# Performance work log

Measured on AMD Instinct MI355X. Metric: run time of the kernel, lower is better.

The kernel has to match this reference:

```python
import jax, jax.numpy as jnp
import numpy as np

B, C, H, W = 4, 64, 64, 64
CQ = C // 2

def setup_inputs() -> dict:
    key = jax.random.key(0)
    ks = jax.random.split(key, 7)
    return {
        "x":  jax.random.normal(ks[0], (B, C, H, W), dtype=jnp.float32),
        "Wq": jax.random.normal(ks[1], (CQ, C), dtype=jnp.float32) * 0.05,
        "bq": jax.random.normal(ks[2], (CQ,), dtype=jnp.float32) * 0.05,
        "Wk": jax.random.normal(ks[3], (CQ, C), dtype=jnp.float32) * 0.05,
        "bk": jax.random.normal(ks[4], (CQ,), dtype=jnp.float32) * 0.05,
        "Wl": jax.random.normal(ks[5], (C, C), dtype=jnp.float32) * 0.05,
        "bl": jax.random.normal(ks[6], (C,), dtype=jnp.float32) * 0.05,
    }

def reference(x, Wq, bq, Wk, bk, Wl, bl):
    b, c, h, w = x.shape
    hw = h * w
    xf = x.reshape(b, c, hw)                                   # [B,C,HW]
    # 1x1 convs == per-pixel linear projections
    q = jnp.einsum('oc,bci->boi', Wq, xf) + bq[None, :, None]  # [B,CQ,HW]
    k = jnp.einsum('oc,bci->boi', Wk, xf) + bk[None, :, None]  # [B,CQ,HW]
    # energy[b,i,j] = <q[:,i], k[:,j]>  (proj_query permuted to [B,HW,CQ])
    energy = jnp.einsum('bci,bcj->bij', q, k)                  # [B,HW,HW]
    attn = jax.nn.softmax(energy, axis=-1)                     # softmax over last dim (keys j)
    # torch.bmm(proj_value, attention): out[b,c,j] = sum_i value[b,c,i] * attn[b,i,j]
    out = jnp.einsum('bci,bij->bcj', xf, attn)                 # [B,C,HW]
    out = out.reshape(b, c, h, w)
    out = jnp.einsum('oc,bchw->bohw', Wl, out) + bl[None, :, None, None]
    return out + x
```

## Files before the change

### kernel.cpp

```cpp
#include <hip/hip_runtime.h>
#include <hip/hip_bf16.h>


#define HW 4096
#define BN 4
#define CD 64
#define ISPL 8
#define LOG2E 1.44269504f

typedef short bf16x8 __attribute__((ext_vector_type(8)));
typedef float f32x4 __attribute__((ext_vector_type(4)));

static __device__ inline unsigned bfbits(float f) {
    union { float f; unsigned u; } v{f};
    return (v.u + 0x8000u) >> 16;
}
static __device__ inline float b2f(short s) {
    unsigned u = ((unsigned)(unsigned short)s) << 16;
    float f; __builtin_memcpy(&f, &u, 4); return f;
}
static __device__ inline int cvtpk(float lo, float hi) {
    __hip_bfloat162 h = __float22bfloat162_rn(make_float2(lo, hi));
    int r; __builtin_memcpy(&r, &h, 4); return r;
}
static __device__ inline void gl16(const void* g, void* l) {
    __builtin_amdgcn_global_load_lds(
        (const __attribute__((address_space(1))) unsigned int*)g,
        (__attribute__((address_space(3))) unsigned int*)l, 16, 0, 0);
}



__global__ __launch_bounds__(256, 4) void k_proj(
    const float* __restrict__ x, const float* __restrict__ Wq, const float* __restrict__ bq,
    const float* __restrict__ Wk, const float* __restrict__ bk, const float* __restrict__ Wl,
    short* __restrict__ Qt, short* __restrict__ Kt, short* __restrict__ Yc)
{
    __shared__ __align__(16) char sm[18944];
    short* WcL   = (short*)sm;
    short* xT    = (short*)(sm + 16384);
    float* biasL = (float*)(sm + 18432);

    int t = threadIdx.x;
    int wv = t >> 6, l = t & 63, g = l >> 4, n = l & 15;

    {
        int row = t >> 1, half = t & 1;
        const float* src; float scale = 1.f;
        if (row < 32)      { src = Wq + row * CD; scale = LOG2E; }
        else if (row < 64) { src = Wk + (row - 32) * CD; }
        else               { src = Wl + (row - 64) * CD; }
        int pk[16];
#pragma unroll
        for (int e = 0; e < 16; ++e)
            pk[e] = cvtpk(src[half * 32 + 2 * e] * scale, src[half * 32 + 2 * e + 1] * scale);
#pragma unroll
        for (int q = 0; q < 4; ++q)
            *(int4*)(WcL + row * 64 + ((((half << 2) + q) ^ (row & 7)) << 3)) =
                make_int4(pk[4 * q], pk[4 * q + 1], pk[4 * q + 2], pk[4 * q + 3]);
        if (half == 0)
            biasL[row] = (row < 32) ? LOG2E * bq[row] : (row < 64) ? bk[row - 32] : 0.f;
    }
    int pix0 = blockIdx.x << 4;
    {
        int c = t >> 2, q = t & 3;
        int b = pix0 >> 12, pxb = pix0 & (HW - 1);
        float4 v = *(const float4*)(x + ((size_t)b << 18) + ((size_t)c << 12) + pxb + q * 4);
        float vv[4] = {v.x, v.y, v.z, v.w};
#pragma unroll
        for (int e = 0; e < 4; ++e) {
            int px = q * 4 + e;
            xT[px * 64 + (((c >> 3) ^ (px & 7)) << 3) + (c & 7)] = (short)bfbits(vv[e]);
        }
    }
    __syncthreads();

    bf16x8 B0 = *(const bf16x8*)(xT + n * 64 + ((g ^ (n & 7)) << 3));
    bf16x8 B1 = *(const bf16x8*)(xT + n * 64 + (((4 + g) ^ (n & 7)) << 3));
    int pg = pix0 + n;
#pragma unroll
    for (int mm = 0; mm < 2; ++mm) {
        int mt = wv * 2 + mm;
        bf16x8 A0 = *(const bf16x8*)(WcL + (mt * 16 + n) * 64 + ((g ^ (n & 7)) << 3));
        bf16x8 A1 = *(const bf16x8*)(WcL + (mt * 16 + n) * 64 + (((4 + g) ^ (n & 7)) << 3));
        f32x4 d = {0.f, 0.f, 0.f, 0.f};
        d = __builtin_amdgcn_mfma_f32_16x16x32_bf16(A0, B0, d, 0, 0, 0);
        d = __builtin_amdgcn_mfma_f32_16x16x32_bf16(A1, B1, d, 0, 0, 0);
        d += *(const f32x4*)(biasL + mt * 16 + g * 4);
        if (mt < 4) {
            short* dst = (mt < 2 ? Qt : Kt) + ((size_t)pg << 5) + ((mt & 1) << 4) + (g << 2);
            *(int2*)dst = make_int2(cvtpk(d[0], d[1]), cvtpk(d[2], d[3]));
        } else {
            int ch2 = (mt - 4) * 16 + g * 4;
            int bb = pg >> 12, ii = pg & (HW - 1);
#pragma unroll
            for (int r = 0; r < 4; ++r)
                Yc[(((size_t)(bb * CD + ch2 + r)) << 12) + ii] = (short)bfbits(d[r]);
        }
    }
}


__global__ __launch_bounds__(256, 4) void k_pass1m(
    const short* __restrict__ Qt, const short* __restrict__ Kt, float* __restrict__ mrow)
{
    __shared__ float red[4][16];
    int t = threadIdx.x;
    int wv = t >> 6, l = t & 63, g = l >> 4, n = l & 15;
    int ch = blockIdx.x;
    int b = ch & 3, i0 = (ch >> 2) * 16;
    size_t bHW = (size_t)b << 12;

    bf16x8 aq = *(const bf16x8*)(Qt + ((bHW + i0 + n) << 5) + (g << 3));
    f32x4 ls = {0.f, 0.f, 0.f, 0.f};
    const short* kbase = Kt + ((bHW + wv * 1024 + n) << 5) + (g << 3);
#pragma unroll 8
    for (int jt = 0; jt < 64; ++jt) {
        bf16x8 bk = *(const bf16x8*)(kbase + jt * 512);
        f32x4 z = {0.f, 0.f, 0.f, 0.f};
        f32x4 s = __builtin_amdgcn_mfma_f32_16x16x32_bf16(aq, bk, z, 0, 0, 0);
        ls[0] += exp2f(s[0]); ls[1] += exp2f(s[1]);
        ls[2] += exp2f(s[2]); ls[3] += exp2f(s[3]);
    }
#pragma unroll
    for (int msk = 1; msk < 16; msk <<= 1) {
        ls[0] += __shfl_xor(ls[0], msk, 64);
        ls[1] += __shfl_xor(ls[1], msk, 64);
        ls[2] += __shfl_xor(ls[2], msk, 64);
        ls[3] += __shfl_xor(ls[3], msk, 64);
    }
    if (n == 0) {
#pragma unroll
        for (int r = 0; r < 4; ++r) red[wv][g * 4 + r] = ls[r];
    }
    __syncthreads();
    if (t < 16) {
        float s = red[0][t] + red[1][t] + red[2][t] + red[3][t];
        mrow[bHW + i0 + t] = -log2f(s);
    }
}


__global__ __launch_bounds__(256, 4) void k_pass2(
    const short* __restrict__ Qt, const short* __restrict__ Kt,
    const short* __restrict__ Yc, const float* __restrict__ mrow,
    short* __restrict__ Opart)
{
    __shared__ __align__(16) char smem[36864];
    short* QtL = (short*)smem;
    short* W2L = (short*)(smem + 8192);
    short* Pb  = (short*)(smem + 24576);
    float* MtA = (float*)(smem + 34816);

    int t = threadIdx.x;
    int wv = t >> 6, l = t & 63, g = l >> 4, n = l & 15;
    int ch = blockIdx.x;
    int b = ch >> 8, isp = (ch >> 5) & 7, jt = ch & 31;
    int j0 = jt * 128 + wv * 32;
    size_t bHW = (size_t)b << 12;
    short* Pw = Pb + wv * 1280;

    bf16x8 bk0 = *(const bf16x8*)(Kt + ((bHW + j0 + n) << 5) + (g << 3));
    bf16x8 bk1 = *(const bf16x8*)(Kt + ((bHW + j0 + 16 + n) << 5) + (g << 3));

    f32x4 oacc[2][4];
#pragma unroll
    for (int a = 0; a < 2; ++a)
#pragma unroll
        for (int m = 0; m < 4; ++m) oacc[a][m] = (f32x4){0.f, 0.f, 0.f, 0.f};

    int swz = ((t & 7) ^ ((t >> 3) & 7)) << 4;
    const char* qsrc = (const char*)Qt + ((bHW + (size_t)isp * 512) << 6) + t * 16;
    const char* wsrc = (const char*)Yc + (((size_t)(b * CD + (t >> 3)) << 12) + isp * 512) * 2 + swz;
    char* qd0 = (char*)QtL + t * 16;  char* qd1 = qd0 + 4096;
    char* wd0 = (char*)W2L + t * 16;  char* wd1 = wd0 + 8192;

    gl16(qsrc, qd0);
    gl16(wsrc, wd0);
    gl16(wsrc + (32ull << 13), wd0 + 4096);
    if (t < 128)
        gl16((const char*)(mrow + bHW + (size_t)isp * 512) + t * 16, (char*)MtA + t * 16);
    asm volatile("s_waitcnt vmcnt(0)" ::: "memory");
    __builtin_amdgcn_s_barrier();
    __builtin_amdgcn_sched_barrier(0);

    const int NT = 8;
    for (int st = 0; st < NT; ++st) {
        int cur = st & 1;
        if (st > 0) {
            __builtin_amdgcn_s_barrier();
            __builtin_amdgcn_sched_barrier(0);
        }
        if (st + 1 < NT) {
            gl16(qsrc + (size_t)(st + 1) * 4096, cur ? qd0 : qd1);
            gl16(wsrc + (size_t)(st + 1) * 128, cur ? wd0 : wd1);
            gl16(wsrc + (size_t)(st + 1) * 128 + (32ull << 13), (cur ? wd0 : wd1) + 4096);
            asm volatile("s_waitcnt vmcnt(3)" ::: "memory");
        } else {
            asm volatile("s_waitcnt vmcnt(0)" ::: "memory");
        }
        __builtin_amdgcn_sched_barrier(0);

        const short* qL = QtL + cur * 2048;
        const char* wL = (const char*)W2L + cur * 8192;
        const float* mL = MtA + st * 64;
#pragma unroll
        for (int ks = 0; ks < 2; ++ks) {
            bf16x8 aq0 = *(const bf16x8*)(qL + (ks * 32 + n) * 32 + g * 8);
            bf16x8 aq1 = *(const bf16x8*)(qL + (ks * 32 + 16 + n) * 32 + g * 8);
            f32x4 cm0 = *(const f32x4*)(mL + ks * 32 + g * 4);
            f32x4 cm1 = *(const f32x4*)(mL + ks * 32 + 16 + g * 4);
            __builtin_amdgcn_s_setprio(1);
            f32x4 s00 = __builtin_amdgcn_mfma_f32_16x16x32_bf16(aq0, bk0, cm0, 0, 0, 0);
            f32x4 s01 = __builtin_amdgcn_mfma_f32_16x16x32_bf16(aq1, bk0, cm1, 0, 0, 0);
            f32x4 s10 = __builtin_amdgcn_mfma_f32_16x16x32_bf16(aq0, bk1, cm0, 0, 0, 0);
            f32x4 s11 = __builtin_amdgcn_mfma_f32_16x16x32_bf16(aq1, bk1, cm1, 0, 0, 0);
            __builtin_amdgcn_s_setprio(0);
            *(int2*)(Pw + n * 40 + 4 * g) =
                make_int2(cvtpk(exp2f(s00[0]), exp2f(s00[1])), cvtpk(exp2f(s00[2]), exp2f(s00[3])));
            *(int2*)(Pw + n * 40 + 16 + 4 * g) =
                make_int2(cvtpk(exp2f(s01[0]), exp2f(s01[1])), cvtpk(exp2f(s01[2]), exp2f(s01[3])));
            *(int2*)(Pw + (16 + n) * 40 + 4 * g) =
                make_int2(cvtpk(exp2f(s10[0]), exp2f(s10[1])), cvtpk(exp2f(s10[2]), exp2f(s10[3])));
            *(int2*)(Pw + (16 + n) * 40 + 16 + 4 * g) =
                make_int2(cvtpk(exp2f(s11[0]), exp2f(s11[1])), cvtpk(exp2f(s11[2]), exp2f(s11[3])));
            bf16x8 pb0 = *(const bf16x8*)(Pw + n * 40 + 8 * g);
            bf16x8 pb1 = *(const bf16x8*)(Pw + (16 + n) * 40 + 8 * g);
            __builtin_amdgcn_s_setprio(1);
#pragma unroll
            for (int mb = 0; mb < 4; ++mb) {
                bf16x8 aw = *(const bf16x8*)(wL + (mb * 16 + n) * 128 + ((((ks << 2) + g) ^ (n & 7)) << 4));
                oacc[0][mb] = __builtin_amdgcn_mfma_f32_16x16x32_bf16(aw, pb0, oacc[0][mb], 0, 0, 0);
                oacc[1][mb] = __builtin_amdgcn_mfma_f32_16x16x32_bf16(aw, pb1, oacc[1][mb], 0, 0, 0);
            }
            __builtin_amdgcn_s_setprio(0);
        }
        __builtin_amdgcn_sched_barrier(0);
    }
    size_t obase = ((((size_t)isp * BN + b) * CD) << 12) + j0 + n;
#pragma unroll
    for (int j2 = 0; j2 < 2; ++j2)
#pragma unroll
        for (int mb = 0; mb < 4; ++mb)
#pragma unroll
            for (int r = 0; r < 4; ++r)
                Opart[obase + (((size_t)(mb * 16 + g * 4 + r)) << 12) + j2 * 16] =
                    (short)bfbits(oacc[j2][mb][r]);
}


__global__ __launch_bounds__(256, 4) void k_merge(
    const short* __restrict__ Opart, const float* __restrict__ x,
    const float* __restrict__ bl, float* __restrict__ out)
{
    int t = threadIdx.x;
    int e = (blockIdx.x * 256 + t) * 4;
    int c = (e >> 12) & 63;
    float4 r = *(const float4*)(x + e);
    float bc = bl[c];
    r.x += bc; r.y += bc; r.z += bc; r.w += bc;
#pragma unroll
    for (int p = 0; p < ISPL; ++p) {
        int2 o4 = *(const int2*)(Opart + ((size_t)p << 20) + e);
        r.x += b2f((short)(o4.x & 0xffff));
        r.y += b2f((short)(o4.x >> 16));
        r.z += b2f((short)(o4.y & 0xffff));
        r.w += b2f((short)(o4.y >> 16));
    }
    *(float4*)(out + e) = r;
}

extern "C" void kernel_launch(void* const* d_in, const int* in_sizes, int n_in,
                              void* d_out, int out_size, void* d_ws, size_t ws_size,
                              hipStream_t stream)
{
    (void)in_sizes; (void)n_in; (void)out_size; (void)ws_size;
    const float* x  = (const float*)d_in[0];
    const float* Wq = (const float*)d_in[1];
    const float* bq = (const float*)d_in[2];
    const float* Wk = (const float*)d_in[3];
    const float* bk = (const float*)d_in[4];
    const float* Wl = (const float*)d_in[5];
    const float* bl = (const float*)d_in[6];
    float* out = (float*)d_out;
    char* base = (char*)d_ws;

    short* Qt    = (short*)(base);
    short* Kt    = (short*)(base + 0x100000);
    short* Yc    = (short*)(base + 0x200000);
    float* mrow  = (float*)(base + 0x500000);
    short* Opart = (short*)(base + 0x510000);

    hipLaunchKernelGGL(k_proj, dim3(1024), dim3(256), 0, stream,
                       x, Wq, bq, Wk, bk, Wl, Qt, Kt, Yc);
    hipLaunchKernelGGL(k_pass1m, dim3(1024), dim3(256), 0, stream, Qt, Kt, mrow);
    hipLaunchKernelGGL(k_pass2, dim3(1024), dim3(256), 0, stream,
                       Qt, Kt, Yc, mrow, Opart);
    hipLaunchKernelGGL(k_merge, dim3(1024), dim3(256), 0, stream, Opart, x, bl, out);
}
```

Baseline: 63.98 us.

## Halve i-split count and double rows per pass1 block to reuse K loads

New measurement: 65.61 us. +2.6%, slower.

```diff
diff --git a/kernel.cpp b/kernel.cpp
--- a/kernel.cpp
+++ b/kernel.cpp
@@ -5,7 +5,7 @@
 #define HW 4096
 #define BN 4
 #define CD 64
-#define ISPL 8
+#define ISPL 4
 #define LOG2E 1.44269504f
 
 typedef short bf16x8 __attribute__((ext_vector_type(8)));
@@ -104,37 +104,45 @@
 __global__ __launch_bounds__(256, 4) void k_pass1m(
     const short* __restrict__ Qt, const short* __restrict__ Kt, float* __restrict__ mrow)
 {
-    __shared__ float red[4][16];
+    __shared__ float red[4][32];
     int t = threadIdx.x;
     int wv = t >> 6, l = t & 63, g = l >> 4, n = l & 15;
     int ch = blockIdx.x;
-    int b = ch & 3, i0 = (ch >> 2) * 16;
+    int b = ch & 3, i0 = (ch >> 2) * 32;
     size_t bHW = (size_t)b << 12;
 
-    bf16x8 aq = *(const bf16x8*)(Qt + ((bHW + i0 + n) << 5) + (g << 3));
-    f32x4 ls = {0.f, 0.f, 0.f, 0.f};
+    bf16x8 aq0 = *(const bf16x8*)(Qt + ((bHW + i0 + n) << 5) + (g << 3));
+    bf16x8 aq1 = *(const bf16x8*)(Qt + ((bHW + i0 + 16 + n) << 5) + (g << 3));
+    f32x4 ls0 = {0.f, 0.f, 0.f, 0.f}, ls1 = {0.f, 0.f, 0.f, 0.f};
     const short* kbase = Kt + ((bHW + wv * 1024 + n) << 5) + (g << 3);
-#pragma unroll 8
+#pragma unroll 4
     for (int jt = 0; jt < 64; ++jt) {
-        bf16x8 bk = *(const bf16x8*)(kbase + jt * 512);
+        bf16x8 bkv = *(const bf16x8*)(kbase + jt * 512);
         f32x4 z = {0.f, 0.f, 0.f, 0.f};
-        f32x4 s = __builtin_amdgcn_mfma_f32_16x16x32_bf16(aq, bk, z, 0, 0, 0);
-        ls[0] += exp2f(s[0]); ls[1] += exp2f(s[1]);
-        ls[2] += exp2f(s[2]); ls[3] += exp2f(s[3]);
+        f32x4 s0 = __builtin_amdgcn_mfma_f32_16x16x32_bf16(aq0, bkv, z, 0, 0, 0);
+        f32x4 s1 = __builtin_amdgcn_mfma_f32_16x16x32_bf16(aq1, bkv, z, 0, 0, 0);
+        ls0[0] += exp2f(s0[0]); ls0[1] += exp2f(s0[1]);
+        ls0[2] += exp2f(s0[2]); ls0[3] += exp2f(s0[3]);
+        ls1[0] += exp2f(s1[0]); ls1[1] += exp2f(s1[1]);
+        ls1[2] += exp2f(s1[2]); ls1[3] += exp2f(s1[3]);
     }
 #pragma unroll
     for (int msk = 1; msk < 16; msk <<= 1) {
-        ls[0] += __shfl_xor(ls[0], msk, 64);
-        ls[1] += __shfl_xor(ls[1], msk, 64);
-        ls[2] += __shfl_xor(ls[2], msk, 64);
-        ls[3] += __shfl_xor(ls[3], msk, 64);
+#pragma unroll
+        for (int r = 0; r < 4; ++r) {
+            ls0[r] += __shfl_xor(ls0[r], msk, 64);
+            ls1[r] += __shfl_xor(ls1[r], msk, 64);
+        }
     }
     if (n == 0) {
 #pragma unroll
-        for (int r = 0; r < 4; ++r) red[wv][g * 4 + r] = ls[r];
+        for (int r = 0; r < 4; ++r) {
+            red[wv][g * 4 + r] = ls0[r];
+            red[wv][16 + g * 4 + r] = ls1[r];
+        }
     }
     __syncthreads();
-    if (t < 16) {
+    if (t < 32) {
         float s = red[0][t] + red[1][t] + red[2][t] + red[3][t];
         mrow[bHW + i0 + t] = -log2f(s);
     }
@@ -146,7 +154,7 @@
     const short* __restrict__ Yc, const float* __restrict__ mrow,
     short* __restrict__ Opart)
 {
-    __shared__ __align__(16) char smem[36864];
+    __shared__ __align__(16) char smem[38912];
     short* QtL = (short*)smem;
     short* W2L = (short*)(smem + 8192);
     short* Pb  = (short*)(smem + 24576);
@@ -155,7 +163,7 @@
     int t = threadIdx.x;
     int wv = t >> 6, l = t & 63, g = l >> 4, n = l & 15;
     int ch = blockIdx.x;
-    int b = ch >> 8, isp = (ch >> 5) & 7, jt = ch & 31;
+    int b = ch >> 7, isp = (ch >> 5) & 3, jt = ch & 31;
     int j0 = jt * 128 + wv * 32;
     size_t bHW = (size_t)b << 12;
     short* Pw = Pb + wv * 1280;
@@ -170,21 +178,20 @@
         for (int m = 0; m < 4; ++m) oacc[a][m] = (f32x4){0.f, 0.f, 0.f, 0.f};
 
     int swz = ((t & 7) ^ ((t >> 3) & 7)) << 4;
-    const char* qsrc = (const char*)Qt + ((bHW + (size_t)isp * 512) << 6) + t * 16;
-    const char* wsrc = (const char*)Yc + (((size_t)(b * CD + (t >> 3)) << 12) + isp * 512) * 2 + swz;
+    const char* qsrc = (const char*)Qt + ((bHW + (size_t)isp * 1024) << 6) + t * 16;
+    const char* wsrc = (const char*)Yc + (((size_t)(b * CD + (t >> 3)) << 12) + isp * 1024) * 2 + swz;
     char* qd0 = (char*)QtL + t * 16;  char* qd1 = qd0 + 4096;
     char* wd0 = (char*)W2L + t * 16;  char* wd1 = wd0 + 8192;
 
     gl16(qsrc, qd0);
     gl16(wsrc, wd0);
     gl16(wsrc + (32ull << 13), wd0 + 4096);
-    if (t < 128)
-        gl16((const char*)(mrow + bHW + (size_t)isp * 512) + t * 16, (char*)MtA + t * 16);
+    gl16((const char*)(mrow + bHW + (size_t)isp * 1024) + t * 16, (char*)MtA + t * 16);
     asm volatile("s_waitcnt vmcnt(0)" ::: "memory");
     __builtin_amdgcn_s_barrier();
     __builtin_amdgcn_sched_barrier(0);
 
-    const int NT = 8;
+    const int NT = 16;
     for (int st = 0; st < NT; ++st) {
         int cur = st & 1;
         if (st > 0) {
@@ -293,8 +300,8 @@
 
     hipLaunchKernelGGL(k_proj, dim3(1024), dim3(256), 0, stream,
                        x, Wq, bq, Wk, bk, Wl, Qt, Kt, Yc);
-    hipLaunchKernelGGL(k_pass1m, dim3(1024), dim3(256), 0, stream, Qt, Kt, mrow);
-    hipLaunchKernelGGL(k_pass2, dim3(1024), dim3(256), 0, stream,
+    hipLaunchKernelGGL(k_pass1m, dim3(512), dim3(256), 0, stream, Qt, Kt, mrow);
+    hipLaunchKernelGGL(k_pass2, dim3(512), dim3(256), 0, stream,
                        Qt, Kt, Yc, mrow, Opart);
     hipLaunchKernelGGL(k_merge, dim3(1024), dim3(256), 0, stream, Opart, x, bl, out);
 }
```

## Tile pass1 over 64 query rows with double-buffered LDS staging of keys

Applied to the files above, without the earlier changes.

Result: slower. 69.33 us (+8.4%).

```diff
diff --git a/kernel.cpp b/kernel.cpp
--- a/kernel.cpp
+++ b/kernel.cpp
@@ -104,38 +104,89 @@
 __global__ __launch_bounds__(256, 4) void k_pass1m(
     const short* __restrict__ Qt, const short* __restrict__ Kt, float* __restrict__ mrow)
 {
-    __shared__ float red[4][16];
+    __shared__ __align__(16) char sm1[33792];
+    short* KL  = (short*)sm1;
+    float* red = (float*)(sm1 + 32768);
+
     int t = threadIdx.x;
     int wv = t >> 6, l = t & 63, g = l >> 4, n = l & 15;
     int ch = blockIdx.x;
-    int b = ch & 3, i0 = (ch >> 2) * 16;
+    int b = ch & 3, i0 = (ch >> 2) << 6;
     size_t bHW = (size_t)b << 12;
 
-    bf16x8 aq = *(const bf16x8*)(Qt + ((bHW + i0 + n) << 5) + (g << 3));
-    f32x4 ls = {0.f, 0.f, 0.f, 0.f};
-    const short* kbase = Kt + ((bHW + wv * 1024 + n) << 5) + (g << 3);
-#pragma unroll 8
-    for (int jt = 0; jt < 64; ++jt) {
-        bf16x8 bk = *(const bf16x8*)(kbase + jt * 512);
-        f32x4 z = {0.f, 0.f, 0.f, 0.f};
-        f32x4 s = __builtin_amdgcn_mfma_f32_16x16x32_bf16(aq, bk, z, 0, 0, 0);
-        ls[0] += exp2f(s[0]); ls[1] += exp2f(s[1]);
-        ls[2] += exp2f(s[2]); ls[3] += exp2f(s[3]);
-    }
-#pragma unroll
-    for (int msk = 1; msk < 16; msk <<= 1) {
-        ls[0] += __shfl_xor(ls[0], msk, 64);
-        ls[1] += __shfl_xor(ls[1], msk, 64);
-        ls[2] += __shfl_xor(ls[2], msk, 64);
-        ls[3] += __shfl_xor(ls[3], msk, 64);
-    }
-    if (n == 0) {
-#pragma unroll
-        for (int r = 0; r < 4; ++r) red[wv][g * 4 + r] = ls[r];
-    }
+    bf16x8 aq[4];
+#pragma unroll
+    for (int it = 0; it < 4; ++it)
+        aq[it] = *(const bf16x8*)(Qt + ((bHW + i0 + it * 16 + n) << 5) + (g << 3));
+
+    const char* ksrc = (const char*)(Kt + (bHW << 5));
+
+    f32x4 ls[4];
+#pragma unroll
+    for (int it = 0; it < 4; ++it) ls[it] = (f32x4){0.f, 0.f, 0.f, 0.f};
+
+#pragma unroll
+    for (int q = 0; q < 4; ++q) {
+        int off = (wv * 4 + q) * 1024 + l * 16;
+        gl16(ksrc + off, (char*)KL + off);
+    }
+    asm volatile("s_waitcnt vmcnt(0)" ::: "memory");
+    __builtin_amdgcn_s_barrier();
+    __builtin_amdgcn_sched_barrier(0);
+
+    const int NCH = 16;
+    for (int chk = 0; chk < NCH; ++chk) {
+        int cur = chk & 1;
+        if (chk > 0) {
+            __builtin_amdgcn_s_barrier();
+            __builtin_amdgcn_sched_barrier(0);
+        }
+        if (chk + 1 < NCH) {
+#pragma unroll
+            for (int q = 0; q < 4; ++q) {
+                int off = (wv * 4 + q) * 1024 + l * 16;
+                gl16(ksrc + (size_t)(chk + 1) * 16384 + off,
+                     (char*)KL + (cur ^ 1) * 16384 + off);
+            }
+            asm volatile("s_waitcnt vmcnt(4)" ::: "memory");
+        } else {
+            asm volatile("s_waitcnt vmcnt(0)" ::: "memory");
+        }
+        __builtin_amdgcn_sched_barrier(0);
+
+        const short* kb = (const short*)((char*)KL + cur * 16384);
+#pragma unroll
+        for (int jj = 0; jj < 4; ++jj) {
+            bf16x8 bkv = *(const bf16x8*)(kb + (((wv * 4 + jj) * 16 + n) << 5) + (g << 3));
+#pragma unroll
+            for (int it = 0; it < 4; ++it) {
+                f32x4 z = {0.f, 0.f, 0.f, 0.f};
+                f32x4 s = __builtin_amdgcn_mfma_f32_16x16x32_bf16(aq[it], bkv, z, 0, 0, 0);
+                ls[it][0] += exp2f(s[0]); ls[it][1] += exp2f(s[1]);
+                ls[it][2] += exp2f(s[2]); ls[it][3] += exp2f(s[3]);
+            }
+        }
+        __builtin_amdgcn_sched_barrier(0);
+    }
+
+#pragma unroll
+    for (int msk = 1; msk < 16; msk <<= 1)
+#pragma unroll
+        for (int it = 0; it < 4; ++it) {
+            ls[it][0] += __shfl_xor(ls[it][0], msk, 64);
+            ls[it][1] += __shfl_xor(ls[it][1], msk, 64);
+            ls[it][2] += __shfl_xor(ls[it][2], msk, 64);
+            ls[it][3] += __shfl_xor(ls[it][3], msk, 64);
+        }
+    if (n == 0)
+#pragma unroll
+        for (int it = 0; it < 4; ++it)
+#pragma unroll
+            for (int r = 0; r < 4; ++r)
+                red[wv * 64 + it * 16 + g * 4 + r] = ls[it][r];
     __syncthreads();
-    if (t < 16) {
-        float s = red[0][t] + red[1][t] + red[2][t] + red[3][t];
+    if (t < 64) {
+        float s = red[t] + red[64 + t] + red[128 + t] + red[192 + t];
         mrow[bHW + i0 + t] = -log2f(s);
     }
 }
@@ -293,7 +344,7 @@
 
     hipLaunchKernelGGL(k_proj, dim3(1024), dim3(256), 0, stream,
                        x, Wq, bq, Wk, bk, Wl, Qt, Kt, Yc);
-    hipLaunchKernelGGL(k_pass1m, dim3(1024), dim3(256), 0, stream, Qt, Kt, mrow);
+    hipLaunchKernelGGL(k_pass1m, dim3(256), dim3(256), 0, stream, Qt, Kt, mrow);
     hipLaunchKernelGGL(k_pass2, dim3(1024), dim3(256), 0, stream,
                        Qt, Kt, Yc, mrow, Opart);
     hipLaunchKernelGGL(k_merge, dim3(1024), dim3(256), 0, stream, Opart, x, bl, out);
```
